# Optimization experiments

Hardware: AMD Instinct MI355X
Metric: run time of the kernel (lower is better)

Reference implementation:

```python
import jax, jax.numpy as jnp
import numpy as np

MARGIN = 0.3
N, D = 8192, 128
NUM_CLASSES = 512


def setup_inputs() -> dict:
    key = jax.random.key(0)
    k1, k2 = jax.random.split(key)
    embeddings = jax.random.normal(k1, (N, D), dtype=jnp.float32)
    targets = jax.random.randint(k2, (N,), 0, NUM_CLASSES, dtype=jnp.int64)
    return {"embeddings": embeddings, "targets": targets}


def reference(embeddings, targets):
    x = embeddings.astype(jnp.float32)
    # pairwise squared-euclidean: ||xi||^2 + ||xj||^2 - 2 xi.xj, clamped then sqrt
    sq = jnp.sum(x * x, axis=1)  # [N]
    dist = sq[:, None] + sq[None, :] - 2.0 * (x @ x.T)
    dist = jnp.sqrt(jnp.clip(dist, 1e-12, None))  # [N, N]

    is_pos = targets[:, None] == targets[None, :]  # includes diagonal, as in torch code

    # batch-hard mining: per-row hardest positive (max) and hardest negative (min)
    dist_ap = jnp.max(jnp.where(is_pos, dist, -jnp.inf), axis=1)
    dist_an = jnp.min(jnp.where(is_pos, jnp.inf, dist), axis=1)

    # MarginRankingLoss(margin)(dist_an, dist_ap, y=1) = mean(relu(margin - (dist_an - dist_ap)))
    loss = jnp.mean(jax.nn.relu(dist_ap - dist_an + MARGIN))
    return loss
```

## Files before the change

kernel.cpp:

```cpp
#include <hip/hip_runtime.h>
#include <hip/hip_bf16.h>

#define N_ROWS 8192
#define DIM 128
#define MARGIN_F 0.3f

typedef __attribute__((ext_vector_type(8))) short short8;
typedef __attribute__((ext_vector_type(4))) float f32x4;
typedef __attribute__((ext_vector_type(4))) int int4v;

__global__ __launch_bounds__(256) void prep_kernel(
    const float* __restrict__ x, const int* __restrict__ tgt,
    unsigned short* __restrict__ xbB, float2* __restrict__ meta,
    int* __restrict__ apb, int* __restrict__ anb) {
  const int w = threadIdx.x >> 6, l = threadIdx.x & 63;
  const int row = blockIdx.x * 4 + w;
  float2 v = reinterpret_cast<const float2*>(x + (size_t)row * DIM)[l];
  __hip_bfloat16 b0 = __float2bfloat16(v.x);
  __hip_bfloat16 b1 = __float2bfloat16(v.y);
  ushort2 st;
  st.x = *reinterpret_cast<unsigned short*>(&b0);
  st.y = *reinterpret_cast<unsigned short*>(&b1);
  const int c16 = row >> 4, l15r = row & 15;
  const int unit = c16 * 256 + (l >> 4) * 64 + ((l >> 2) & 3) * 16 + l15r;
  reinterpret_cast<ushort2*>(xbB)[unit * 4 + (l & 3)] = st;

  float s = v.x * v.x + v.y * v.y;
  #pragma unroll
  for (int off = 32; off >= 1; off >>= 1) s += __shfl_xor(s, off);
  if (l == 0) {
    float2 m;
    m.x = s;
    m.y = __int_as_float(tgt[row]);
    meta[row] = m;
    apb[row] = 0x00000000;
    anb[row] = 0x7f800000;
  }
}

__global__ __launch_bounds__(256, 3) void gram_mine_kernel(
    const unsigned short* __restrict__ xbB, const float2* __restrict__ meta,
    int* __restrict__ apb, int* __restrict__ anb) {
  const int t = threadIdx.x;
  const int w = t >> 6, l = t & 63;
  const int l15 = l & 15, l4 = l >> 4;
  const int rb = blockIdx.x * 128 + w * 32;
  const int chunk = blockIdx.y * 256;

  const short8* xf = reinterpret_cast<const short8*>(xbB);

  short8 a0[4], a1[4];
  #pragma unroll
  for (int kk = 0; kk < 4; ++kk) {
    a0[kk] = xf[(rb >> 4) * 256 + kk * 64 + l];
    a1[kk] = xf[((rb >> 4) + 1) * 256 + kk * 64 + l];
  }

  int t_r[8];
  #pragma unroll
  for (int rf = 0; rf < 2; ++rf)
    #pragma unroll
    for (int rg = 0; rg < 4; ++rg)
      t_r[rf * 4 + rg] = __float_as_int(meta[rb + rf * 16 + l4 * 4 + rg].y);

  float ap2[8], an2[8];
  #pragma unroll
  for (int i = 0; i < 8; ++i) { ap2[i] = -__builtin_inff(); an2[i] = __builtin_inff(); }

  short8 bb[2][4];
  float2 mc[4];
  const int cb0 = chunk >> 4;
  #pragma unroll
  for (int cf = 0; cf < 4; ++cf) {
    bb[0][cf] = xf[(cb0 + cf) * 256 + l];
    mc[cf] = meta[chunk + cf * 16 + l15];
  }

  #pragma unroll
  for (int ct = 0; ct < 4; ++ct) {
    const int cb16 = (chunk >> 4) + ct * 4;
    const int nt = (ct < 3) ? (ct + 1) : 3;
    const int nb16 = (chunk >> 4) + nt * 4;

    f32x4 acc[2][4];
    #pragma unroll
    for (int rf = 0; rf < 2; ++rf)
      #pragma unroll
      for (int cf = 0; cf < 4; ++cf) acc[rf][cf] = (f32x4){0.f, 0.f, 0.f, 0.f};

    float2 mn[4];
    #pragma unroll
    for (int kk = 0; kk < 4; ++kk) {
      if (kk < 3) {
        #pragma unroll
        for (int cf = 0; cf < 4; ++cf)
          bb[(kk + 1) & 1][cf] = xf[(cb16 + cf) * 256 + (kk + 1) * 64 + l];
      } else {
        #pragma unroll
        for (int cf = 0; cf < 4; ++cf)
          bb[0][cf] = xf[(nb16 + cf) * 256 + l];
        #pragma unroll
        for (int cf = 0; cf < 4; ++cf)
          mn[cf] = meta[chunk + nt * 64 + cf * 16 + l15];
      }
      #pragma unroll
      for (int cf = 0; cf < 4; ++cf) {
        acc[0][cf] = __builtin_amdgcn_mfma_f32_16x16x32_bf16(
            a0[kk], bb[kk & 1][cf], acc[0][cf], 0, 0, 0);
        acc[1][cf] = __builtin_amdgcn_mfma_f32_16x16x32_bf16(
            a1[kk], bb[kk & 1][cf], acc[1][cf], 0, 0, 0);
      }
    }

    #pragma unroll
    for (int cf = 0; cf < 4; ++cf) {
      const float sqc = mc[cf].x;
      const int tc = __float_as_int(mc[cf].y);
      #pragma unroll
      for (int rf = 0; rf < 2; ++rf)
        #pragma unroll
        for (int rg = 0; rg < 4; ++rg) {
          int idx = rf * 4 + rg;
          float v = fmaf(-2.f, acc[rf][cf][rg], sqc);
          bool pos = (t_r[idx] == tc);
          ap2[idx] = pos ? fmaxf(ap2[idx], v) : ap2[idx];
          an2[idx] = pos ? an2[idx] : fminf(an2[idx], v);
        }
    }
    #pragma unroll
    for (int cf = 0; cf < 4; ++cf) mc[cf] = mn[cf];
  }

  #pragma unroll
  for (int i = 0; i < 8; ++i) {
    #pragma unroll
    for (int off = 1; off < 16; off <<= 1) {
      ap2[i] = fmaxf(ap2[i], __shfl_xor(ap2[i], off));
      an2[i] = fminf(an2[i], __shfl_xor(an2[i], off));
    }
  }
  if (l15 == 0) {
    #pragma unroll
    for (int rf = 0; rf < 2; ++rf)
      #pragma unroll
      for (int rg = 0; rg < 4; ++rg) {
        int row = rb + rf * 16 + l4 * 4 + rg;
        float sqr = meta[row].x;
        float a2 = fmaxf(ap2[rf * 4 + rg] + sqr, 1e-12f);
        float n2 = fmaxf(an2[rf * 4 + rg] + sqr, 1e-12f);
        atomicMax(apb + row, __float_as_int(a2));
        atomicMin(anb + row, __float_as_int(n2));
      }
  }
}

__global__ __launch_bounds__(1024) void loss_kernel(
    const int4v* __restrict__ apb, const int4v* __restrict__ anb,
    float* __restrict__ out) {
  __shared__ float red[16];
  float s = 0.f;
  for (int i = threadIdx.x; i < N_ROWS / 4; i += 1024) {
    int4v a4 = apb[i], n4 = anb[i];
    #pragma unroll
    for (int j = 0; j < 4; ++j) {
      float ap = sqrtf(__int_as_float(a4[j]));
      float an = sqrtf(__int_as_float(n4[j]));
      float li = ap - an + MARGIN_F;
      s += li > 0.f ? li : 0.f;
    }
  }
  #pragma unroll
  for (int off = 32; off >= 1; off >>= 1) s += __shfl_xor(s, off);
  const int w = threadIdx.x >> 6, l = threadIdx.x & 63;
  if (l == 0) red[w] = s;
  __syncthreads();
  if (threadIdx.x < 16) {
    float v = red[threadIdx.x];
    #pragma unroll
    for (int off = 8; off >= 1; off >>= 1) v += __shfl_xor(v, off);
    if (threadIdx.x == 0) out[0] = v / (float)N_ROWS;
  }
}

extern "C" void kernel_launch(void* const* d_in, const int* in_sizes, int n_in,
                              void* d_out, int out_size, void* d_ws, size_t ws_size,
                              hipStream_t stream) {
  const float* x = (const float*)d_in[0];
  const int* tgt = (const int*)d_in[1];
  float* out = (float*)d_out;

  char* ws = (char*)d_ws;
  unsigned short* xbB = (unsigned short*)ws;
  float2* meta = (float2*)(ws + 2097152);
  int* apb = (int*)(ws + 2097152 + 65536);
  int* anb = (int*)(ws + 2097152 + 65536 + 32768);

  prep_kernel<<<2048, 256, 0, stream>>>(x, tgt, xbB, meta, apb, anb);
  gram_mine_kernel<<<dim3(64, 32), 256, 0, stream>>>(xbB, meta, apb, anb);
  loss_kernel<<<1, 1024, 0, stream>>>((const int4v*)apb, (const int4v*)anb, out);
}
```

Measured before the change: 48.66 us.

## Exploit distance symmetry by computing only upper-triangular Gram tiles

Replaces the full 64x32 grid of row-block by 256-column tiles with a triangular enumeration of 128x128 tiles (2080 blocks). Off-diagonal tiles mine both the row direction and the transposed column direction, reducing column-side results with cross-lane shuffles and column atomics. This roughly halves the MFMA work, at the cost of an extra epilogue reduction, more atomics, and a sqrt-based block index decode.

```diff
diff --git a/kernel.cpp b/kernel.cpp
--- a/kernel.cpp
+++ b/kernel.cpp
@@ -44,8 +44,18 @@
   const int t = threadIdx.x;
   const int w = t >> 6, l = t & 63;
   const int l15 = l & 15, l4 = l >> 4;
-  const int rb = blockIdx.x * 128 + w * 32;
-  const int chunk = blockIdx.y * 256;
+
+  const int NT = 64;
+  const int id = blockIdx.x;
+  int bi = (int)((2.0f * NT + 1.0f -
+                  sqrtf((2.0f * NT + 1.0f) * (2.0f * NT + 1.0f) - 8.0f * (float)id)) * 0.5f);
+  while ((bi + 1) * NT - ((bi + 1) * bi) / 2 <= id) ++bi;
+  while (bi * NT - (bi * (bi - 1)) / 2 > id) --bi;
+  const int bj = bi + (id - (bi * NT - (bi * (bi - 1)) / 2));
+  const bool offd = (bi != bj);
+
+  const int rb = bi * 128 + w * 32;
+  const int cbase = bj * 128;
 
   const short8* xf = reinterpret_cast<const short8*>(xbB);
 
@@ -56,12 +66,15 @@
     a1[kk] = xf[((rb >> 4) + 1) * 256 + kk * 64 + l];
   }
 
-  int t_r[8];
+  float sq_r[8]; int t_r[8];
   #pragma unroll
   for (int rf = 0; rf < 2; ++rf)
     #pragma unroll
-    for (int rg = 0; rg < 4; ++rg)
-      t_r[rf * 4 + rg] = __float_as_int(meta[rb + rf * 16 + l4 * 4 + rg].y);
+    for (int rg = 0; rg < 4; ++rg) {
+      float2 m = meta[rb + rf * 16 + l4 * 4 + rg];
+      sq_r[rf * 4 + rg] = m.x;
+      t_r[rf * 4 + rg] = __float_as_int(m.y);
+    }
 
   float ap2[8], an2[8];
   #pragma unroll
@@ -69,18 +82,18 @@
 
   short8 bb[2][4];
   float2 mc[4];
-  const int cb0 = chunk >> 4;
+  const int cb0 = cbase >> 4;
   #pragma unroll
   for (int cf = 0; cf < 4; ++cf) {
     bb[0][cf] = xf[(cb0 + cf) * 256 + l];
-    mc[cf] = meta[chunk + cf * 16 + l15];
-  }
-
-  #pragma unroll
-  for (int ct = 0; ct < 4; ++ct) {
-    const int cb16 = (chunk >> 4) + ct * 4;
-    const int nt = (ct < 3) ? (ct + 1) : 3;
-    const int nb16 = (chunk >> 4) + nt * 4;
+    mc[cf] = meta[cbase + cf * 16 + l15];
+  }
+
+  #pragma unroll
+  for (int st = 0; st < 2; ++st) {
+    const int cb16 = (cbase >> 4) + st * 4;
+    const int ns = (st < 1) ? 1 : 1;
+    const int nb16 = (cbase >> 4) + ns * 4;
 
     f32x4 acc[2][4];
     #pragma unroll
@@ -101,7 +114,7 @@
           bb[0][cf] = xf[(nb16 + cf) * 256 + l];
         #pragma unroll
         for (int cf = 0; cf < 4; ++cf)
-          mn[cf] = meta[chunk + nt * 64 + cf * 16 + l15];
+          mn[cf] = meta[cbase + ns * 64 + cf * 16 + l15];
       }
       #pragma unroll
       for (int cf = 0; cf < 4; ++cf) {
@@ -116,16 +129,34 @@
     for (int cf = 0; cf < 4; ++cf) {
       const float sqc = mc[cf].x;
       const int tc = __float_as_int(mc[cf].y);
+      float apc = -__builtin_inff(), anc = __builtin_inff();
       #pragma unroll
       for (int rf = 0; rf < 2; ++rf)
         #pragma unroll
         for (int rg = 0; rg < 4; ++rg) {
           int idx = rf * 4 + rg;
-          float v = fmaf(-2.f, acc[rf][cf][rg], sqc);
+          float s2 = acc[rf][cf][rg];
+          float v = fmaf(-2.f, s2, sqc);
+          float u = fmaf(-2.f, s2, sq_r[idx]);
           bool pos = (t_r[idx] == tc);
           ap2[idx] = pos ? fmaxf(ap2[idx], v) : ap2[idx];
           an2[idx] = pos ? an2[idx] : fminf(an2[idx], v);
+          apc = pos ? fmaxf(apc, u) : apc;
+          anc = pos ? anc : fminf(anc, u);
         }
+      if (offd) {
+        apc = fmaxf(apc, __shfl_xor(apc, 16));
+        apc = fmaxf(apc, __shfl_xor(apc, 32));
+        anc = fminf(anc, __shfl_xor(anc, 16));
+        anc = fminf(anc, __shfl_xor(anc, 32));
+        if (l4 == 0) {
+          int colg = cbase + st * 64 + cf * 16 + l15;
+          float a2 = fmaxf(apc + sqc, 1e-12f);
+          float n2 = fmaxf(anc + sqc, 1e-12f);
+          atomicMax(apb + colg, __float_as_int(a2));
+          atomicMin(anb + colg, __float_as_int(n2));
+        }
+      }
     }
     #pragma unroll
     for (int cf = 0; cf < 4; ++cf) mc[cf] = mn[cf];
@@ -196,6 +227,6 @@
   int* anb = (int*)(ws + 2097152 + 65536 + 32768);
 
   prep_kernel<<<2048, 256, 0, stream>>>(x, tgt, xbB, meta, apb, anb);
-  gram_mine_kernel<<<dim3(64, 32), 256, 0, stream>>>(xbB, meta, apb, anb);
+  gram_mine_kernel<<<2080, 256, 0, stream>>>(xbB, meta, apb, anb);
   loss_kernel<<<1, 1024, 0, stream>>>((const int4v*)apb, (const int4v*)anb, out);
 }
```

After: 62.73 us. +28.9%, slower.
